# Kernel tuning notes

Hardware: AMD Instinct MI355X
Metric: run time of the kernel (lower is better)

Reference implementation:

```python
import jax, jax.numpy as jnp
import numpy as np

T_GRID = 2048  # static grid size (= density * data range 128)
EPS = 1e-8


def rbf(x1, x2, ls, os_):
    # x1: [B,N,1], x2: [B,M,1] -> [B,N,M]; gpytorch ScaleKernel(RBFKernel())
    d2 = (x1 - jnp.swapaxes(x2, -1, -2)) ** 2
    return os_ * jnp.exp(-0.5 * d2 / (ls * ls))


def conv1d(x, w, b):
    # x: [B,C,T], w: [O,I,5], pad 2 -> same length
    y = jax.lax.conv_general_dilated(x, w, (1,), [(2, 2)],
                                     dimension_numbers=('NCH', 'OIH', 'NCH'))
    return y + b[None, :, None]


def setup_inputs() -> dict:
    key = jax.random.key(0)
    ks = jax.random.split(key, 12)
    B, Nc, Nt = 16, 2048, 2048
    xc = jax.random.uniform(ks[0], (B, Nc, 1), jnp.float32) * 128.0
    yc = jax.random.normal(ks[1], (B, Nc, 1), jnp.float32)
    xt = jax.random.uniform(ks[2], (B, Nt, 1), jnp.float32) * 128.0
    ln2 = float(np.log(2.0))  # softplus(0), gpytorch default raw param init
    params = {
        'ls_psi': jnp.float32(ln2), 'os_psi': jnp.float32(ln2),
        'ls_rho': jnp.float32(ln2), 'os_rho': jnp.float32(ln2),
        'w1': jax.random.normal(ks[3], (16, 3, 5), jnp.float32) * 0.2,
        'b1': jnp.zeros((16,), jnp.float32),
        'w2': jax.random.normal(ks[4], (32, 16, 5), jnp.float32) * 0.1,
        'b2': jnp.zeros((32,), jnp.float32),
        'w3': jax.random.normal(ks[5], (16, 32, 5), jnp.float32) * 0.1,
        'b3': jnp.zeros((16,), jnp.float32),
        'w4': jax.random.normal(ks[6], (2, 16, 5), jnp.float32) * 0.1,
        'b4': jnp.zeros((2,), jnp.float32),
    }
    return {'xc': xc, 'yc': yc, 'xt': xt, **params}


def reference(xc, yc, xt, ls_psi, os_psi, ls_rho, os_rho,
              w1, b1, w2, b2, w3, b3, w4, b4):
    B = xc.shape[0]
    lower = jnp.minimum(xc.min(), xt.min())
    upper = jnp.maximum(xc.max(), xt.max())
    t = jnp.linspace(lower, upper, T_GRID)                      # [T]
    t = jnp.broadcast_to(t[None, :, None], (B, T_GRID, 1))      # [B,T,1]

    # SetConv encoder: h = psi(t, xc) @ phi(yc), phi = [y^0, y^1]
    Kt = rbf(t, xc, ls_psi, os_psi)                             # [B,T,Nc]
    phi = jnp.concatenate([jnp.ones_like(yc), yc], -1)          # [B,Nc,2]
    h = jnp.matmul(Kt, phi)                                     # [B,T,2]
    h0, h1 = h[..., :1], h[..., 1:]
    h1 = h1 / (h0 + EPS)
    rep = jnp.concatenate([t, h0, h1], -1).swapaxes(-1, -2)     # [B,3,T]

    # small Conv1d decoder stack
    f = jax.nn.relu(conv1d(rep, w1, b1))
    f = jax.nn.relu(conv1d(f, w2, b2))
    f = jax.nn.relu(conv1d(f, w3, b3))
    f = conv1d(f, w4, b4).swapaxes(-1, -2)                      # [B,T,2]
    f_mu, f_sigma = f[..., :1], f[..., 1:]

    # SetConv decoder onto targets
    Kr = rbf(xt, t, ls_rho, os_rho)                             # [B,Nt,T]
    mu = jnp.matmul(Kr, f_mu)                                   # [B,Nt,1]
    sigma = jnp.matmul(Kr, jax.nn.softplus(f_sigma))            # [B,Nt,1]
    return jnp.concatenate([mu, sigma], -1)                     # [B,Nt,2]
```

## Files before the change

kernel.cpp:

```cpp
#include <hip/hip_runtime.h>
#include <math.h>

#define T_GRID 2048
#define NC 2048
#define NT 2048
#define BATCH 16
#define NBINS 256
#define CAP2 1024
#define XCUT 28.0f

__device__ __forceinline__ int bin_of(float v, float lower, float invbinw) {
    int b = (int)floorf((v - lower) * invbinw);
    return min(NBINS - 1, max(0, b));
}

__global__ __launch_bounds__(1024) void k_minmax(const float4* __restrict__ xc4,
                                                 const float4* __restrict__ xt4,
                                                 float* __restrict__ mm) {
    float lo = 3.4e38f, hi = -3.4e38f;
    for (int i = threadIdx.x; i < BATCH * NC / 4; i += 1024) {
        float4 v = xc4[i];
        lo = fminf(lo, fminf(fminf(v.x, v.y), fminf(v.z, v.w)));
        hi = fmaxf(hi, fmaxf(fmaxf(v.x, v.y), fmaxf(v.z, v.w)));
    }
    for (int i = threadIdx.x; i < BATCH * NT / 4; i += 1024) {
        float4 v = xt4[i];
        lo = fminf(lo, fminf(fminf(v.x, v.y), fminf(v.z, v.w)));
        hi = fmaxf(hi, fmaxf(fmaxf(v.x, v.y), fmaxf(v.z, v.w)));
    }
    for (int off = 32; off; off >>= 1) {
        lo = fminf(lo, __shfl_down(lo, off));
        hi = fmaxf(hi, __shfl_down(hi, off));
    }
    __shared__ float slo[16], shi[16];
    int lane = threadIdx.x & 63, wv = threadIdx.x >> 6;
    if (lane == 0) { slo[wv] = lo; shi[wv] = hi; }
    __syncthreads();
    if (threadIdx.x == 0) {
        for (int w = 1; w < 16; w++) { lo = fminf(lo, slo[w]); hi = fmaxf(hi, shi[w]); }
        mm[0] = lo; mm[1] = hi;
    }
}

__global__ __launch_bounds__(256) void k_binsort(const float* __restrict__ xc,
                                                 const float* __restrict__ yc,
                                                 const float* __restrict__ mm,
                                                 int* __restrict__ starts,
                                                 float2* __restrict__ sorted) {
    __shared__ int hist[NBINS];
    __shared__ int cur[NBINS];
    __shared__ int sc[NBINS];
    int b = blockIdx.x, tid = threadIdx.x;
    float lower = mm[0], upper = mm[1];
    float invbinw = (float)NBINS / (upper - lower);
    float xv[8], yv[8];
    int bn[8];
    hist[tid] = 0;
    __syncthreads();
#pragma unroll
    for (int k = 0; k < 8; k++) {
        int idx = tid + 256 * k;
        xv[k] = xc[b * NC + idx];
        yv[k] = yc[b * NC + idx];
        bn[k] = bin_of(xv[k], lower, invbinw);
        atomicAdd(&hist[bn[k]], 1);
    }
    __syncthreads();
    int v = hist[tid];
    sc[tid] = v;
    __syncthreads();
    for (int off = 1; off < NBINS; off <<= 1) {
        int t = (tid >= off) ? sc[tid - off] : 0;
        __syncthreads();
        sc[tid] += t;
        __syncthreads();
    }
    int excl = sc[tid] - v;
    starts[b * (NBINS + 1) + tid] = excl;
    cur[tid] = excl;
    if (tid == NBINS - 1) starts[b * (NBINS + 1) + NBINS] = sc[tid];
    __syncthreads();
#pragma unroll
    for (int k = 0; k < 8; k++) {
        int pos = atomicAdd(&cur[bn[k]], 1);
        sorted[b * NC + pos] = make_float2(xv[k], yv[k]);
    }
}

#define TILE 112
#define BW 132

__global__ __launch_bounds__(256) void k_conv(const float* __restrict__ mm,
                                              const float2* __restrict__ sorted,
                                              const int* __restrict__ starts,
                                              const float* __restrict__ ls_psi,
                                              const float* __restrict__ os_psi,
                                              const float* __restrict__ w1, const float* __restrict__ b1,
                                              const float* __restrict__ w2, const float* __restrict__ b2,
                                              const float* __restrict__ w3, const float* __restrict__ b3,
                                              const float* __restrict__ w4, const float* __restrict__ b4,
                                              float* __restrict__ f) {
    __shared__ float rep[3][BW];
    __shared__ float L1[16][BW];
    __shared__ float L2[32][BW];
    __shared__ float L3[16][BW];
    __shared__ float w1L[15][16];
    __shared__ float w2L[80][32];
    __shared__ float w3L[160][16];
    __shared__ float w4L[80][2];
    __shared__ float bL[66];
    __shared__ float2 sxy[CAP2];

    int tid = threadIdx.x;
    int b = blockIdx.y;
    int gstart = blockIdx.x * TILE - 8;

    float lower = mm[0], upper = mm[1];
    float step = (upper - lower) * (1.0f / (T_GRID - 1));
    float invbinw = (float)NBINS / (upper - lower);
    float ls = ls_psi[0], os = os_psi[0];
    float c2 = -0.72134752044f / (ls * ls);
    float R = ls * sqrtf(XCUT);

    for (int idx = tid; idx < 240; idx += 256)  { int o = idx / 15,  r2 = idx % 15;  w1L[r2][o] = w1[idx]; }
    for (int idx = tid; idx < 2560; idx += 256) { int o = idx / 80,  r2 = idx % 80;  w2L[r2][o] = w2[idx]; }
    for (int idx = tid; idx < 2560; idx += 256) { int o = idx / 160, r2 = idx % 160; w3L[r2][o] = w3[idx]; }
    for (int idx = tid; idx < 160; idx += 256)  { int o = idx / 80,  r2 = idx % 80;  w4L[r2][o] = w4[idx]; }
    if (tid < 16) bL[tid] = b1[tid];
    if (tid < 32) bL[16 + tid] = b2[tid];
    if (tid < 16) bL[48 + tid] = b3[tid];
    if (tid < 2)  bL[64 + tid] = b4[tid];
    if (tid < 4) {
        int c = (tid < 2) ? tid : tid + 128;
        for (int r2 = 0; r2 < 3; r2++)  rep[r2][c] = 0.f;
        for (int r2 = 0; r2 < 16; r2++) { L1[r2][c] = 0.f; L3[r2][c] = 0.f; }
        for (int r2 = 0; r2 < 32; r2++) L2[r2][c] = 0.f;
    }

    {
        int p = tid & 127, r = tid >> 7;
        int gp = gstart + p;
        bool pvalid = (gp >= 0 && gp < T_GRID);
        float t = fmaf((float)gp, step, lower);
        const int* sb = starts + b * (NBINS + 1);
        const float2* srt = sorted + b * NC;
        int my_lo = 0, my_hi = 0;
        if (pvalid) {
            my_lo = sb[bin_of(t - R, lower, invbinw)];
            my_hi = sb[bin_of(t + R, lower, invbinw) + 1];
        }
        int g0 = max(gstart, 0), g1 = min(gstart + 127, T_GRID - 1);
        float tmin = fmaf((float)g0, step, lower) - R;
        float tmax = fmaf((float)g1, step, lower) + R;
        int u_lo = sb[bin_of(tmin, lower, invbinw)];
        int u_hi = sb[bin_of(tmax, lower, invbinw) + 1];

        float S0 = 0.f, S1 = 0.f;
        for (int base = u_lo; base < u_hi; base += CAP2) {
            int n = min(CAP2, u_hi - base);
            __syncthreads();
            for (int k = tid; k < n; k += 256) sxy[k] = srt[base + k];
            __syncthreads();
            int aa = max(my_lo, base) - base;
            int ee = min(my_hi, base + n) - base;
            for (int j = aa + r; j < ee; j += 2) {
                float2 xy = sxy[j];
                float d = t - xy.x;
                float ev = exp2f(d * d * c2);
                S0 += ev;
                S1 = fmaf(ev, xy.y, S1);
            }
        }
        __syncthreads();
        float2* part = sxy;
        part[tid] = make_float2(S0, S1);
        __syncthreads();
        if (tid < 128) {
            float2 q = part[tid + 128];
            S0 += q.x; S1 += q.y;
            float h0 = os * S0;
            float h1 = os * S1 / (h0 + 1e-8f);
            rep[0][p + 2] = pvalid ? t : 0.f;
            rep[1][p + 2] = pvalid ? h0 : 0.f;
            rep[2][p + 2] = pvalid ? h1 : 0.f;
        }
    }
    __syncthreads();

    {
        int o = tid & 15, s0 = (tid >> 4) << 3;
        float acc[8];
        float bias = bL[o];
#pragma unroll
        for (int s = 0; s < 8; s++) acc[s] = bias;
        for (int i = 0; i < 3; i++) {
            float x[12];
#pragma unroll
            for (int j = 0; j < 12; j++) x[j] = rep[i][s0 + j];
#pragma unroll
            for (int k = 0; k < 5; k++) {
                float w = w1L[i * 5 + k][o];
#pragma unroll
                for (int s = 0; s < 8; s++) acc[s] = fmaf(x[s + k], w, acc[s]);
            }
        }
#pragma unroll
        for (int s = 0; s < 8; s++) {
            int p = s0 + s, gp = gstart + p;
            bool vv = (p >= 2 && p < 126 && gp >= 0 && gp < T_GRID);
            L1[o][p + 2] = vv ? fmaxf(acc[s], 0.f) : 0.f;
        }
    }
    __syncthreads();

    {
        int o = tid & 31, s0 = (tid >> 5) << 4;
        float acc[16];
        float bias = bL[16 + o];
#pragma unroll
        for (int s = 0; s < 16; s++) acc[s] = bias;
        for (int i = 0; i < 16; i++) {
            float x[20];
#pragma unroll
            for (int j = 0; j < 20; j++) x[j] = L1[i][s0 + j];
#pragma unroll
            for (int k = 0; k < 5; k++) {
                float w = w2L[i * 5 + k][o];
#pragma unroll
                for (int s = 0; s < 16; s++) acc[s] = fmaf(x[s + k], w, acc[s]);
            }
        }
#pragma unroll
        for (int s = 0; s < 16; s++) {
            int p = s0 + s, gp = gstart + p;
            bool vv = (p >= 4 && p < 124 && gp >= 0 && gp < T_GRID);
            L2[o][p + 2] = vv ? fmaxf(acc[s], 0.f) : 0.f;
        }
    }
    __syncthreads();

    {
        int o = tid & 15, s0 = (tid >> 4) << 3;
        float acc[8];
        float bias = bL[48 + o];
#pragma unroll
        for (int s = 0; s < 8; s++) acc[s] = bias;
        for (int i = 0; i < 32; i++) {
            float x[12];
#pragma unroll
            for (int j = 0; j < 12; j++) x[j] = L2[i][s0 + j];
#pragma unroll
            for (int k = 0; k < 5; k++) {
                float w = w3L[i * 5 + k][o];
#pragma unroll
                for (int s = 0; s < 8; s++) acc[s] = fmaf(x[s + k], w, acc[s]);
            }
        }
#pragma unroll
        for (int s = 0; s < 8; s++) {
            int p = s0 + s, gp = gstart + p;
            bool vv = (p >= 6 && p < 122 && gp >= 0 && gp < T_GRID);
            L3[o][p + 2] = vv ? fmaxf(acc[s], 0.f) : 0.f;
        }
    }
    __syncthreads();

    {
        int o = tid & 1, p = tid >> 1;
        float a = bL[64 + o];
        for (int i = 0; i < 16; i++) {
#pragma unroll
            for (int k = 0; k < 5; k++) {
                a = fmaf(L3[i][p + k], w4L[i * 5 + k][o], a);
            }
        }
        int gp = gstart + p;
        if (p >= 8 && p < 120 && gp >= 0 && gp < T_GRID) {
            if (o) {
                float sp = fmaxf(a, 0.f) + log1pf(expf(-fabsf(a)));
                f[2 * (b * T_GRID + gp) + 1] = sp;
            } else {
                f[2 * (b * T_GRID + gp)] = a;
            }
        }
    }
}

__global__ __launch_bounds__(256) void k_out(const float* __restrict__ xt,
                                             const float* __restrict__ ls_rho,
                                             const float* __restrict__ os_rho,
                                             const float* __restrict__ mm,
                                             const float2* __restrict__ f,
                                             float2* __restrict__ out) {
    __shared__ float2 sf[T_GRID];
    __shared__ float2 part[256];
    int b = blockIdx.y, tid = threadIdx.x;
    int it = blockIdx.x * 64 + (tid & 63);
    int r = tid >> 6;
    float lower = mm[0], upper = mm[1];
    float step = (upper - lower) * (1.0f / (T_GRID - 1));
    float invstep = 1.0f / step;
    float ls = ls_rho[0], os = os_rho[0];
    float c2 = -0.72134752044f / (ls * ls);
    float R = ls * sqrtf(XCUT);
    float x = xt[b * NT + it];

    const float2* fb = f + b * T_GRID;
    for (int k = tid; k < T_GRID; k += 256) sf[k] = fb[k];
    __syncthreads();

    int j0 = max(0, (int)floorf((x - R - lower) * invstep));
    int j1 = min(T_GRID - 1, (int)ceilf((x + R - lower) * invstep));

    float Smu = 0.f, Ssg = 0.f;
    float jf = (float)(j0 + r);
    for (int j = j0 + r; j <= j1; j += 4) {
        float2 v = sf[j];
        float d = x - fmaf(jf, step, lower);
        float e = exp2f(d * d * c2);
        Smu = fmaf(e, v.x, Smu);
        Ssg = fmaf(e, v.y, Ssg);
        jf += 4.0f;
    }
    part[tid] = make_float2(Smu, Ssg);
    __syncthreads();
    if (r == 0) {
#pragma unroll
        for (int q = 64; q < 256; q += 64) {
            float2 pp = part[tid + q];
            Smu += pp.x; Ssg += pp.y;
        }
        out[b * NT + it] = make_float2(os * Smu, os * Ssg);
    }
}

extern "C" void kernel_launch(void* const* d_in, const int* in_sizes, int n_in,
                              void* d_out, int out_size, void* d_ws, size_t ws_size,
                              hipStream_t stream) {
    const float* xc = (const float*)d_in[0];
    const float* yc = (const float*)d_in[1];
    const float* xt = (const float*)d_in[2];
    const float* ls_psi = (const float*)d_in[3];
    const float* os_psi = (const float*)d_in[4];
    const float* ls_rho = (const float*)d_in[5];
    const float* os_rho = (const float*)d_in[6];
    const float* w1 = (const float*)d_in[7];
    const float* b1 = (const float*)d_in[8];
    const float* w2 = (const float*)d_in[9];
    const float* b2 = (const float*)d_in[10];
    const float* w3 = (const float*)d_in[11];
    const float* b3 = (const float*)d_in[12];
    const float* w4 = (const float*)d_in[13];
    const float* b4 = (const float*)d_in[14];

    char* ws = (char*)d_ws;
    float* mm     = (float*)ws;
    int* starts   = (int*)(ws + 64);
    float2* sorted= (float2*)(ws + 16640);
    float* f      = (float*)(ws + 278912);

    k_minmax<<<dim3(1), dim3(1024), 0, stream>>>((const float4*)xc, (const float4*)xt, mm);

    k_binsort<<<dim3(BATCH), dim3(256), 0, stream>>>(xc, yc, mm, starts, sorted);

    int ntiles = (T_GRID + TILE - 1) / TILE;
    k_conv<<<dim3(ntiles, BATCH), dim3(256), 0, stream>>>(mm, sorted, starts,
                                                          ls_psi, os_psi,
                                                          w1, b1, w2, b2, w3, b3, w4, b4, f);

    k_out<<<dim3(NT / 64, BATCH), dim3(256), 0, stream>>>(xt, ls_rho, os_rho, mm,
                                                          (const float2*)f, (float2*)d_out);
}
```

Measured before the change: 124.0 us.

## Fuse min/max and binning into conv kernel with per-tile local bucketing

Removes the separate min/max and global bin-sort kernels. Each conv block now recomputes the global min/max redundantly by scanning all xc/xt values, then buckets only the context points within its tile's cutoff window into shared memory. Shared memory is reused via a pool overlapping the point buffer with L2/L3 activations, which cuts the LDS footprint. The cost is that every block reads all 64K inputs for the reduction, and points beyond a fixed PCAP of 768 are silently dropped.

```diff
diff --git a/kernel.cpp b/kernel.cpp
--- a/kernel.cpp
+++ b/kernel.cpp
@@ -5,122 +5,41 @@
 #define NC 2048
 #define NT 2048
 #define BATCH 16
-#define NBINS 256
-#define CAP2 1024
 #define XCUT 28.0f
-
-__device__ __forceinline__ int bin_of(float v, float lower, float invbinw) {
-    int b = (int)floorf((v - lower) * invbinw);
-    return min(NBINS - 1, max(0, b));
-}
-
-__global__ __launch_bounds__(1024) void k_minmax(const float4* __restrict__ xc4,
-                                                 const float4* __restrict__ xt4,
-                                                 float* __restrict__ mm) {
-    float lo = 3.4e38f, hi = -3.4e38f;
-    for (int i = threadIdx.x; i < BATCH * NC / 4; i += 1024) {
-        float4 v = xc4[i];
-        lo = fminf(lo, fminf(fminf(v.x, v.y), fminf(v.z, v.w)));
-        hi = fmaxf(hi, fmaxf(fmaxf(v.x, v.y), fmaxf(v.z, v.w)));
-    }
-    for (int i = threadIdx.x; i < BATCH * NT / 4; i += 1024) {
-        float4 v = xt4[i];
-        lo = fminf(lo, fminf(fminf(v.x, v.y), fminf(v.z, v.w)));
-        hi = fmaxf(hi, fmaxf(fmaxf(v.x, v.y), fmaxf(v.z, v.w)));
-    }
-    for (int off = 32; off; off >>= 1) {
-        lo = fminf(lo, __shfl_down(lo, off));
-        hi = fmaxf(hi, __shfl_down(hi, off));
-    }
-    __shared__ float slo[16], shi[16];
-    int lane = threadIdx.x & 63, wv = threadIdx.x >> 6;
-    if (lane == 0) { slo[wv] = lo; shi[wv] = hi; }
-    __syncthreads();
-    if (threadIdx.x == 0) {
-        for (int w = 1; w < 16; w++) { lo = fminf(lo, slo[w]); hi = fmaxf(hi, shi[w]); }
-        mm[0] = lo; mm[1] = hi;
-    }
-}
-
-__global__ __launch_bounds__(256) void k_binsort(const float* __restrict__ xc,
-                                                 const float* __restrict__ yc,
-                                                 const float* __restrict__ mm,
-                                                 int* __restrict__ starts,
-                                                 float2* __restrict__ sorted) {
-    __shared__ int hist[NBINS];
-    __shared__ int cur[NBINS];
-    __shared__ int sc[NBINS];
-    int b = blockIdx.x, tid = threadIdx.x;
-    float lower = mm[0], upper = mm[1];
-    float invbinw = (float)NBINS / (upper - lower);
-    float xv[8], yv[8];
-    int bn[8];
-    hist[tid] = 0;
-    __syncthreads();
-#pragma unroll
-    for (int k = 0; k < 8; k++) {
-        int idx = tid + 256 * k;
-        xv[k] = xc[b * NC + idx];
-        yv[k] = yc[b * NC + idx];
-        bn[k] = bin_of(xv[k], lower, invbinw);
-        atomicAdd(&hist[bn[k]], 1);
-    }
-    __syncthreads();
-    int v = hist[tid];
-    sc[tid] = v;
-    __syncthreads();
-    for (int off = 1; off < NBINS; off <<= 1) {
-        int t = (tid >= off) ? sc[tid - off] : 0;
-        __syncthreads();
-        sc[tid] += t;
-        __syncthreads();
-    }
-    int excl = sc[tid] - v;
-    starts[b * (NBINS + 1) + tid] = excl;
-    cur[tid] = excl;
-    if (tid == NBINS - 1) starts[b * (NBINS + 1) + NBINS] = sc[tid];
-    __syncthreads();
-#pragma unroll
-    for (int k = 0; k < 8; k++) {
-        int pos = atomicAdd(&cur[bn[k]], 1);
-        sorted[b * NC + pos] = make_float2(xv[k], yv[k]);
-    }
-}
-
 #define TILE 112
 #define BW 132
-
-__global__ __launch_bounds__(256) void k_conv(const float* __restrict__ mm,
-                                              const float2* __restrict__ sorted,
-                                              const int* __restrict__ starts,
-                                              const float* __restrict__ ls_psi,
-                                              const float* __restrict__ os_psi,
-                                              const float* __restrict__ w1, const float* __restrict__ b1,
-                                              const float* __restrict__ w2, const float* __restrict__ b2,
-                                              const float* __restrict__ w3, const float* __restrict__ b3,
-                                              const float* __restrict__ w4, const float* __restrict__ b4,
-                                              float* __restrict__ f) {
+#define PCAP 768
+#define NSB 32
+
+__global__ __launch_bounds__(256) void k_fused(
+        const float4* __restrict__ xc4, const float4* __restrict__ xt4,
+        const float* __restrict__ xc, const float* __restrict__ yc,
+        const float* __restrict__ ls_psi, const float* __restrict__ os_psi,
+        const float* __restrict__ w1, const float* __restrict__ b1,
+        const float* __restrict__ w2, const float* __restrict__ b2,
+        const float* __restrict__ w3, const float* __restrict__ b3,
+        const float* __restrict__ w4, const float* __restrict__ b4,
+        float* __restrict__ mm, float* __restrict__ f) {
     __shared__ float rep[3][BW];
-    __shared__ float L1[16][BW];
-    __shared__ float L2[32][BW];
-    __shared__ float L3[16][BW];
+    __shared__ float L1s[16][BW];
+    __shared__ __align__(16) char pool[32 * BW * 4];
     __shared__ float w1L[15][16];
     __shared__ float w2L[80][32];
     __shared__ float w3L[160][16];
     __shared__ float w4L[80][2];
     __shared__ float bL[66];
-    __shared__ float2 sxy[CAP2];
+
+    float (*L2s)[BW] = reinterpret_cast<float (*)[BW]>(pool);
+    float (*L3s)[BW] = L1s;
+    float2* pts    = reinterpret_cast<float2*>(pool);
+    float2* part   = reinterpret_cast<float2*>(pool + 6144);
+    int*    bstart = reinterpret_cast<int*>(pool + 8192);
+    int*    curi   = reinterpret_cast<int*>(pool + 8336);
+    float*  bc     = reinterpret_cast<float*>(pool + 8464);
 
     int tid = threadIdx.x;
     int b = blockIdx.y;
     int gstart = blockIdx.x * TILE - 8;
-
-    float lower = mm[0], upper = mm[1];
-    float step = (upper - lower) * (1.0f / (T_GRID - 1));
-    float invbinw = (float)NBINS / (upper - lower);
-    float ls = ls_psi[0], os = os_psi[0];
-    float c2 = -0.72134752044f / (ls * ls);
-    float R = ls * sqrtf(XCUT);
 
     for (int idx = tid; idx < 240; idx += 256)  { int o = idx / 15,  r2 = idx % 15;  w1L[r2][o] = w1[idx]; }
     for (int idx = tid; idx < 2560; idx += 256) { int o = idx / 80,  r2 = idx % 80;  w2L[r2][o] = w2[idx]; }
@@ -133,46 +52,103 @@
     if (tid < 4) {
         int c = (tid < 2) ? tid : tid + 128;
         for (int r2 = 0; r2 < 3; r2++)  rep[r2][c] = 0.f;
-        for (int r2 = 0; r2 < 16; r2++) { L1[r2][c] = 0.f; L3[r2][c] = 0.f; }
-        for (int r2 = 0; r2 < 32; r2++) L2[r2][c] = 0.f;
-    }
-
-    {
-        int p = tid & 127, r = tid >> 7;
+        for (int r2 = 0; r2 < 16; r2++) L1s[r2][c] = 0.f;
+    }
+
+    float lo = 3.4e38f, hi = -3.4e38f;
+    for (int i = tid; i < BATCH * NC / 4; i += 256) {
+        float4 v = xc4[i];
+        lo = fminf(lo, fminf(fminf(v.x, v.y), fminf(v.z, v.w)));
+        hi = fmaxf(hi, fmaxf(fmaxf(v.x, v.y), fmaxf(v.z, v.w)));
+    }
+    for (int i = tid; i < BATCH * NT / 4; i += 256) {
+        float4 v = xt4[i];
+        lo = fminf(lo, fminf(fminf(v.x, v.y), fminf(v.z, v.w)));
+        hi = fmaxf(hi, fmaxf(fmaxf(v.x, v.y), fmaxf(v.z, v.w)));
+    }
+    for (int off = 32; off; off >>= 1) {
+        lo = fminf(lo, __shfl_down(lo, off));
+        hi = fmaxf(hi, __shfl_down(hi, off));
+    }
+    if ((tid & 63) == 0) part[tid >> 6] = make_float2(lo, hi);
+    __syncthreads();
+    if (tid == 0) {
+        for (int w = 1; w < 4; w++) {
+            float2 q = part[w];
+            lo = fminf(lo, q.x); hi = fmaxf(hi, q.y);
+        }
+        bc[0] = lo; bc[1] = hi;
+        mm[0] = lo; mm[1] = hi;
+    }
+    __syncthreads();
+    float lower = bc[0], upper = bc[1];
+    float step = (upper - lower) * (1.0f / (T_GRID - 1));
+    float ls = ls_psi[0], os = os_psi[0];
+    float c2 = -0.72134752044f / (ls * ls);
+    float R = ls * sqrtf(XCUT);
+
+    int g0 = max(gstart, 0), g1 = min(gstart + 127, T_GRID - 1);
+    float tmin = fmaf((float)g0, step, lower) - R;
+    float tmax = fmaf((float)g1, step, lower) + R;
+    float sbw_inv = (float)NSB / (tmax - tmin);
+
+    if (tid < NSB + 1) bstart[tid] = 0;
+    __syncthreads();
+    float xv[8], yv[8];
+    int bn[8];
+    const float* xb = xc + b * NC;
+    const float* yb = yc + b * NC;
+#pragma unroll
+    for (int k = 0; k < 8; k++) {
+        int idx = tid + 256 * k;
+        xv[k] = xb[idx];
+        yv[k] = yb[idx];
+        bool in = (xv[k] >= tmin) & (xv[k] <= tmax);
+        bn[k] = -1;
+        if (in) {
+            bn[k] = min(NSB - 1, max(0, (int)((xv[k] - tmin) * sbw_inv)));
+            atomicAdd(&bstart[bn[k]], 1);
+        }
+    }
+    __syncthreads();
+    if (tid == 0) {
+        int run = 0;
+        for (int i = 0; i < NSB; i++) { int c = bstart[i]; bstart[i] = run; run += c; }
+        bstart[NSB] = run;
+    }
+    __syncthreads();
+    if (tid < NSB) curi[tid] = bstart[tid];
+    __syncthreads();
+#pragma unroll
+    for (int k = 0; k < 8; k++) {
+        if (bn[k] >= 0) {
+            int pos = atomicAdd(&curi[bn[k]], 1);
+            if (pos < PCAP) pts[pos] = make_float2(xv[k], yv[k]);
+        }
+    }
+    __syncthreads();
+
+    {
+        int p = tid & 127, rr = tid >> 7;
         int gp = gstart + p;
         bool pvalid = (gp >= 0 && gp < T_GRID);
         float t = fmaf((float)gp, step, lower);
-        const int* sb = starts + b * (NBINS + 1);
-        const float2* srt = sorted + b * NC;
-        int my_lo = 0, my_hi = 0;
+        int s = 0, e = 0;
         if (pvalid) {
-            my_lo = sb[bin_of(t - R, lower, invbinw)];
-            my_hi = sb[bin_of(t + R, lower, invbinw) + 1];
-        }
-        int g0 = max(gstart, 0), g1 = min(gstart + 127, T_GRID - 1);
-        float tmin = fmaf((float)g0, step, lower) - R;
-        float tmax = fmaf((float)g1, step, lower) + R;
-        int u_lo = sb[bin_of(tmin, lower, invbinw)];
-        int u_hi = sb[bin_of(tmax, lower, invbinw) + 1];
-
+            int b0 = min(NSB - 1, max(0, (int)((t - R - tmin) * sbw_inv)));
+            int b1 = min(NSB - 1, max(0, (int)((t + R - tmin) * sbw_inv)));
+            s = bstart[b0];
+            e = min(bstart[b1 + 1], PCAP);
+        }
         float S0 = 0.f, S1 = 0.f;
-        for (int base = u_lo; base < u_hi; base += CAP2) {
-            int n = min(CAP2, u_hi - base);
-            __syncthreads();
-            for (int k = tid; k < n; k += 256) sxy[k] = srt[base + k];
-            __syncthreads();
-            int aa = max(my_lo, base) - base;
-            int ee = min(my_hi, base + n) - base;
-            for (int j = aa + r; j < ee; j += 2) {
-                float2 xy = sxy[j];
-                float d = t - xy.x;
-                float ev = exp2f(d * d * c2);
-                S0 += ev;
-                S1 = fmaf(ev, xy.y, S1);
-            }
+        for (int j = s + rr; j < e; j += 2) {
+            float2 xy = pts[j];
+            float d = t - xy.x;
+            float ev = exp2f(d * d * c2);
+            S0 += ev;
+            S1 = fmaf(ev, xy.y, S1);
         }
         __syncthreads();
-        float2* part = sxy;
         part[tid] = make_float2(S0, S1);
         __syncthreads();
         if (tid < 128) {
@@ -188,6 +164,10 @@
     __syncthreads();
 
     {
+        if (tid < 4) {
+            int c = (tid < 2) ? tid : tid + 128;
+            for (int r2 = 0; r2 < 32; r2++) L2s[r2][c] = 0.f;
+        }
         int o = tid & 15, s0 = (tid >> 4) << 3;
         float acc[8];
         float bias = bL[o];
@@ -204,11 +184,12 @@
                 for (int s = 0; s < 8; s++) acc[s] = fmaf(x[s + k], w, acc[s]);
             }
         }
+        __syncthreads();
 #pragma unroll
         for (int s = 0; s < 8; s++) {
             int p = s0 + s, gp = gstart + p;
             bool vv = (p >= 2 && p < 126 && gp >= 0 && gp < T_GRID);
-            L1[o][p + 2] = vv ? fmaxf(acc[s], 0.f) : 0.f;
+            L1s[o][p + 2] = vv ? fmaxf(acc[s], 0.f) : 0.f;
         }
     }
     __syncthreads();
@@ -222,7 +203,7 @@
         for (int i = 0; i < 16; i++) {
             float x[20];
 #pragma unroll
-            for (int j = 0; j < 20; j++) x[j] = L1[i][s0 + j];
+            for (int j = 0; j < 20; j++) x[j] = L1s[i][s0 + j];
 #pragma unroll
             for (int k = 0; k < 5; k++) {
                 float w = w2L[i * 5 + k][o];
@@ -234,7 +215,7 @@
         for (int s = 0; s < 16; s++) {
             int p = s0 + s, gp = gstart + p;
             bool vv = (p >= 4 && p < 124 && gp >= 0 && gp < T_GRID);
-            L2[o][p + 2] = vv ? fmaxf(acc[s], 0.f) : 0.f;
+            L2s[o][p + 2] = vv ? fmaxf(acc[s], 0.f) : 0.f;
         }
     }
     __syncthreads();
@@ -248,7 +229,7 @@
         for (int i = 0; i < 32; i++) {
             float x[12];
 #pragma unroll
-            for (int j = 0; j < 12; j++) x[j] = L2[i][s0 + j];
+            for (int j = 0; j < 12; j++) x[j] = L2s[i][s0 + j];
 #pragma unroll
             for (int k = 0; k < 5; k++) {
                 float w = w3L[i * 5 + k][o];
@@ -256,11 +237,12 @@
                 for (int s = 0; s < 8; s++) acc[s] = fmaf(x[s + k], w, acc[s]);
             }
         }
+        __syncthreads();
 #pragma unroll
         for (int s = 0; s < 8; s++) {
             int p = s0 + s, gp = gstart + p;
             bool vv = (p >= 6 && p < 122 && gp >= 0 && gp < T_GRID);
-            L3[o][p + 2] = vv ? fmaxf(acc[s], 0.f) : 0.f;
+            L3s[o][p + 2] = vv ? fmaxf(acc[s], 0.f) : 0.f;
         }
     }
     __syncthreads();
@@ -271,7 +253,7 @@
         for (int i = 0; i < 16; i++) {
 #pragma unroll
             for (int k = 0; k < 5; k++) {
-                a = fmaf(L3[i][p + k], w4L[i * 5 + k][o], a);
+                a = fmaf(L3s[i][p + k], w4L[i * 5 + k][o], a);
             }
         }
         int gp = gstart + p;
@@ -354,20 +336,14 @@
     const float* b4 = (const float*)d_in[14];
 
     char* ws = (char*)d_ws;
-    float* mm     = (float*)ws;
-    int* starts   = (int*)(ws + 64);
-    float2* sorted= (float2*)(ws + 16640);
-    float* f      = (float*)(ws + 278912);
-
-    k_minmax<<<dim3(1), dim3(1024), 0, stream>>>((const float4*)xc, (const float4*)xt, mm);
-
-    k_binsort<<<dim3(BATCH), dim3(256), 0, stream>>>(xc, yc, mm, starts, sorted);
+    float* mm = (float*)ws;
+    float* f  = (float*)(ws + 64);
 
     int ntiles = (T_GRID + TILE - 1) / TILE;
-    k_conv<<<dim3(ntiles, BATCH), dim3(256), 0, stream>>>(mm, sorted, starts,
-                                                          ls_psi, os_psi,
-                                                          w1, b1, w2, b2, w3, b3, w4, b4, f);
-
-    k_out<<<dim3(NT / 64, BATCH), dim3(256), 0, stream>>>(xt, ls_rho, os_rho, mm,
-                                                          (const float2*)f, (float2*)d_out);
+    k_fused<<<dim3(ntiles, BATCH), dim3(256), 0, stream>>>(
+        (const float4*)xc, (const float4*)xt, xc, yc, ls_psi, os_psi,
+        w1, b1, w2, b2, w3, b3, w4, b4, mm, f);
+
+    k_out<<<dim3(NT / 64, BATCH), dim3(256), 0, stream>>>(
+        xt, ls_rho, os_rho, mm, (const float2*)f, (float2*)d_out);
 }
```

After: 130.2 us. +5.0%, slower.
